# Optimization experiments

Measured on AMD Instinct MI355X. Metric: run time of the kernel, lower is better.

The kernel has to match this reference:

```python
import jax, jax.numpy as jnp
import numpy as np
import itertools

N_PARTICLES = 8388608
GRID_RES = 2048
BOX_SIZE = 1000.0

def _rotations_47():
    perms = list(itertools.permutations([0, 1, 2]))
    signs = list(itertools.product([1, -1], repeat=3))
    mats = []
    for s in signs:
        for p in perms:
            M = np.zeros((3, 3), np.float32)
            M[0, p[0]] = s[0]; M[1, p[1]] = s[1]; M[2, p[2]] = s[2]
            mats.append(M)
    return jnp.asarray(np.stack(mats)[1:])  # drop identity -> 47 matrices

# Analytic stand-ins for jax_cosmo background quantities (EdS-like forms).
def _Gp(a):
    return a ** 1.5

def _dGfa(a):
    return 1.5 * jnp.sqrt(a)

def _a_of_chi(chi):
    return 1.0 / (1.0 + chi / 3000.0)

def _paint_2d(pos, center, width, box_size, res):
    """CIC scatter of particles inside a z-slab onto a [res,res] density plane."""
    z = pos[:, 2]
    sel = ((z >= center - width * 0.5) & (z < center + width * 0.5)).astype(pos.dtype)
    xy = pos[:, :2] * (res / box_size)          # grid coordinates, [N,2]
    i0 = jnp.floor(xy)
    f = xy - i0                                  # CIC fractional offsets
    i0 = i0.astype(jnp.int32)
    ix0 = jnp.mod(i0[:, 0], res); iy0 = jnp.mod(i0[:, 1], res)
    ix1 = jnp.mod(i0[:, 0] + 1, res); iy1 = jnp.mod(i0[:, 1] + 1, res)
    fx, fy = f[:, 0], f[:, 1]
    flat = jnp.zeros((res * res,), dtype=pos.dtype)
    flat = flat.at[ix0 * res + iy0].add(sel * (1 - fx) * (1 - fy))
    flat = flat.at[ix1 * res + iy0].add(sel * fx * (1 - fy))
    flat = flat.at[ix0 * res + iy1].add(sel * (1 - fx) * fy)
    flat = flat.at[ix1 * res + iy1].add(sel * fx * fy)
    return flat.reshape(res, res)

def setup_inputs():
    key = jax.random.key(0)
    k1, k2 = jax.random.split(key)
    positions = jax.random.uniform(k1, (N_PARTICLES, 3), jnp.float32) * BOX_SIZE
    velocities = jax.random.normal(k2, (N_PARTICLES, 3), jnp.float32) * 2.0
    return {
        "positions": positions,
        "velocities": velocities,
        "rotations": _rotations_47(),
        "observer": jnp.zeros((3,), jnp.float32),
        "r_centers": jnp.asarray([250.0, 750.0, 1250.0, 1750.0], jnp.float32),
        "density_widths": jnp.full((4,), 500.0, jnp.float32),
        "t": jnp.float32(0.8),
        "max_comoving_distance": jnp.float32(BOX_SIZE),
        "box_size": jnp.float32(BOX_SIZE),
        "shell_idx": 2,
        "rotation_idx": 1,
        "grid_res": GRID_RES,
    }

def reference(positions, velocities, rotations, observer, r_centers, density_widths,
              t, max_comoving_distance, box_size, shell_idx, rotation_idx, grid_res):
    r_center = r_centers[shell_idx]
    width = density_widths[shell_idx]
    inside_box = r_center + width * 0.5 <= max_comoving_distance

    def inside_branch(args):
        pos, _vel = args
        return _paint_2d(pos, r_center, width, box_size, grid_res)

    def telephoto_branch(args):
        pos, vel = args
        M = rotations[rotation_idx % 47]                                   # [3,3]
        shift = jnp.floor(r_center / max_comoving_distance) * max_comoving_distance
        p_rot = (pos - observer) @ M.T                                      # rotate about observer
        z_axis = jnp.array([0.0, 0.0, 1.0], pos.dtype)
        p_shift = p_rot + z_axis * shift
        v_rot = vel @ M.T
        dist = jnp.linalg.norm(p_shift - observer, axis=-1)                 # [N]
        a_tgt = _a_of_chi(dist)[:, None]                                    # per-particle target scale factor
        ac = jnp.sqrt(t * a_tgt)
        drift = (_Gp(a_tgt) - _Gp(t)) / _dGfa(ac)
        p_drift = p_shift + drift * v_rot
        return _paint_2d(p_drift + observer, r_center, width, box_size, grid_res)

    return jax.lax.cond(inside_box, inside_branch, telephoto_branch, (positions, velocities))
```

## Files before the change

kernel.cpp:

```cpp
#include <hip/hip_runtime.h>
#include <cmath>


#define TSZ    128
#define NBKT   256
#define NXCC   8
#define CAP    4096
#define DEPTH  32
#define NTH    256
#define NBLK   1024
#define VEC    4
#define DESCMAX 512

typedef float vf4 __attribute__((ext_vector_type(4)));

__device__ __forceinline__ int get_xcc_id() {
    int x = __builtin_amdgcn_s_getreg((3 << 11) | (0 << 6) | 20);
    return x & (NXCC - 1);
}

__device__ __forceinline__ float fast_rcp(float x)  { return __builtin_amdgcn_rcpf(x); }
__device__ __forceinline__ float fast_sqrt(float x) { return __builtin_amdgcn_sqrtf(x); }

__device__ __forceinline__ int wrap_idx(int v, int res) {
    v += (v < 0) ? res : 0;
    v += (v < 0) ? res : 0;
    v += (v < 0) ? res : 0;
    v -= (v >= res) ? res : 0;
    v -= (v >= res) ? res : 0;
    v -= (v >= res) ? res : 0;
    if (v < 0 || v >= res) { v %= res; if (v < 0) v += res; }
    return v;
}

__device__ __forceinline__ void scatter_direct(float* __restrict__ out, int res,
                                               int gx0, int gy0, float fx, float fy) {
    int gx1 = gx0 + 1; if (gx1 >= res) gx1 = 0;
    int gy1 = gy0 + 1; if (gy1 >= res) gy1 = 0;
    atomicAdd(&out[gx0 * res + gy0], (1.0f - fx) * (1.0f - fy));
    atomicAdd(&out[gx1 * res + gy0], fx * (1.0f - fy));
    atomicAdd(&out[gx0 * res + gy1], (1.0f - fx) * fy);
    atomicAdd(&out[gx1 * res + gy1], fx * fy);
}

__device__ __forceinline__ void rec_decode(unsigned rec, int b, int tiles,
                                           int& gx, int& gy, float& fx, float& fy) {
    int tx = b / tiles, ty = b - tx * tiles;
    gx = (tx << 7) + (int)(rec >> 25);
    gy = (ty << 7) + (int)((rec >> 18) & 127u);
    fx = (float)((rec >> 9) & 511u) * (1.0f / 512.0f);
    fy = (float)(rec & 511u) * (1.0f / 512.0f);
}

struct Uni {
    float m00, m01, m02, m10, m11, m12, m20, m21, m22;
    float ox, oy, oz, shift;
    float r_lo, r_hi, t, gp_t, scale;
    int   resm1, res, tiles;
    bool  inside;
};

__device__ __forceinline__ void tp_process(
    const Uni& u, float px, float py, float pz, float vx, float vy, float vz,
    unsigned* __restrict__ fill, unsigned* __restrict__ buf,
    float* __restrict__ out)
{
    float X, Y, Z;
    if (u.inside) {
        X = px; Y = py; Z = pz;
    } else {
        const float qx_ = px - u.ox, qy_ = py - u.oy, qz_ = pz - u.oz;
        float rx = u.m00 * qx_ + u.m01 * qy_ + u.m02 * qz_;
        float ry = u.m10 * qx_ + u.m11 * qy_ + u.m12 * qz_;
        float rz = u.m20 * qx_ + u.m21 * qy_ + u.m22 * qz_ + u.shift;

        const float vrx = u.m00 * vx + u.m01 * vy + u.m02 * vz;
        const float vry = u.m10 * vx + u.m11 * vy + u.m12 * vz;
        const float vrz = u.m20 * vx + u.m21 * vy + u.m22 * vz;

        const float dx = rx - u.ox, dy = ry - u.oy, dz = rz - u.oz;
        const float dist  = fast_sqrt(dx * dx + dy * dy + dz * dz);
        const float a_tgt = fast_rcp(1.0f + dist * (1.0f / 3000.0f));
        const float ac    = fast_sqrt(u.t * a_tgt);
        const float gp_a  = a_tgt * fast_sqrt(a_tgt);
        const float drift = (gp_a - u.gp_t) * fast_rcp(1.5f * fast_sqrt(ac));

        X = rx + drift * vrx + u.ox;
        Y = ry + drift * vry + u.oy;
        Z = rz + drift * vrz + u.oz;
    }
    if (!(Z >= u.r_lo && Z < u.r_hi)) return;

    const float gx = X * u.scale, gy = Y * u.scale;
    const float fgx = floorf(gx), fgy = floorf(gy);
    const float fx = gx - fgx, fy = gy - fgy;
    const int ix0 = ((int)fgx) & u.resm1;
    const int iy0 = ((int)fgy) & u.resm1;
    const int st = (ix0 >> 7) * u.tiles + (iy0 >> 7);

    unsigned qx = (unsigned)(fx * 512.0f + 0.5f); if (qx > 511u) qx = 511u;
    unsigned qy = (unsigned)(fy * 512.0f + 0.5f); if (qy > 511u) qy = 511u;
    const unsigned rec = ((unsigned)(ix0 & 127) << 25) | ((unsigned)(iy0 & 127) << 18)
                       | (qx << 9) | qy;

    unsigned p = atomicAdd(&fill[st], 1u);
    if (p < DEPTH) buf[st * DEPTH + p] = rec;
    else { atomicSub(&fill[st], 1u); scatter_direct(out, u.res, ix0, iy0, fx, fy); }
}

__global__ __launch_bounds__(NTH) void tp_bin(
    const float* __restrict__ pos, const float* __restrict__ vel,
    const float* __restrict__ rotations, const float* __restrict__ observer,
    const float* __restrict__ r_centers, const float* __restrict__ widths,
    const float* __restrict__ t_p, const float* __restrict__ maxd_p,
    const float* __restrict__ box_p, const int* __restrict__ shell_p,
    const int* __restrict__ ridx_p,
    unsigned* __restrict__ gcnt, unsigned* __restrict__ grec,
    float* __restrict__ out, int res, int tiles, int n, int rounds)
{
    __shared__ unsigned fill[NBKT];
    __shared__ unsigned buf[NBKT * DEPTH];
    __shared__ unsigned descB[DESCMAX];
    __shared__ unsigned descD[DESCMAX];
    __shared__ unsigned ndesc;

    const int tid = threadIdx.x;
    for (int b = tid; b < NBKT; b += NTH) fill[b] = 0;
    if (tid == 0) ndesc = 0;

    Uni u;
    {
        const int   shell    = shell_p[0];
        const float r_center = r_centers[shell];
        const float width    = widths[shell];
        const float maxd     = maxd_p[0];
        const float box      = box_p[0];
        u.t      = t_p[0];
        u.inside = (r_center + width * 0.5f) <= maxd;
        int ridx = ridx_p[0] % 47; if (ridx < 0) ridx += 47;
        const float* M = rotations + 9 * ridx;
        u.m00 = M[0]; u.m01 = M[1]; u.m02 = M[2];
        u.m10 = M[3]; u.m11 = M[4]; u.m12 = M[5];
        u.m20 = M[6]; u.m21 = M[7]; u.m22 = M[8];
        u.ox = observer[0]; u.oy = observer[1]; u.oz = observer[2];
        u.shift = floorf(r_center / maxd) * maxd;
        u.r_lo = r_center - width * 0.5f;
        u.r_hi = r_center + width * 0.5f;
        u.gp_t = u.t * sqrtf(u.t);
        u.scale = (float)res / box;
        u.resm1 = res - 1; u.res = res; u.tiles = tiles;
    }

    const int xcc = get_xcc_id();
    const int segbase = xcc * NBKT;
    const vf4* __restrict__ pos4 = (const vf4*)pos;
    const vf4* __restrict__ vel4 = (const vf4*)vel;

    __syncthreads();

    for (int r = 0; r < rounds; ++r) {
        const int base = ((r * NBLK + blockIdx.x) * NTH + tid) * VEC;
        if (base + VEC <= n) {
            const int q = base * 3 / 4;
            const vf4 a = __builtin_nontemporal_load(pos4 + q);
            const vf4 b = __builtin_nontemporal_load(pos4 + q + 1);
            const vf4 c = __builtin_nontemporal_load(pos4 + q + 2);
            if (u.inside) {
                tp_process(u, a.x, a.y, a.z, 0, 0, 0, fill, buf, out);
                tp_process(u, a.w, b.x, b.y, 0, 0, 0, fill, buf, out);
                tp_process(u, b.z, b.w, c.x, 0, 0, 0, fill, buf, out);
                tp_process(u, c.y, c.z, c.w, 0, 0, 0, fill, buf, out);
            } else {
                const vf4 d = __builtin_nontemporal_load(vel4 + q);
                const vf4 e = __builtin_nontemporal_load(vel4 + q + 1);
                const vf4 f = __builtin_nontemporal_load(vel4 + q + 2);
                tp_process(u, a.x, a.y, a.z, d.x, d.y, d.z, fill, buf, out);
                tp_process(u, a.w, b.x, b.y, d.w, e.x, e.y, fill, buf, out);
                tp_process(u, b.z, b.w, c.x, e.z, e.w, f.x, fill, buf, out);
                tp_process(u, c.y, c.z, c.w, f.y, f.z, f.w, fill, buf, out);
            }
        } else {
            for (int p = 0; p < VEC; ++p) {
                const int i = base + p;
                if (i < n)
                    tp_process(u, pos[3 * i], pos[3 * i + 1], pos[3 * i + 2],
                               vel[3 * i], vel[3 * i + 1], vel[3 * i + 2],
                               fill, buf, out);
            }
        }
        __syncthreads();
        if (tid < NBKT) {
            const unsigned c = fill[tid];
            const unsigned k = c >> 4;
            if (k) {
                unsigned gbase = atomicAdd(&gcnt[segbase + tid], 16u * k);
                unsigned d = atomicAdd(&ndesc, k);
                for (unsigned g = 0; g < k; ++g) {
                    descB[d + g] = (unsigned)tid | ((g * 16u) << 16);
                    descD[d + g] = gbase + 16u * g;
                }
            }
        }
        __syncthreads();
        const unsigned nd = ndesc;
        for (unsigned did = (unsigned)(tid >> 4); did < nd; did += NTH / 16) {
            const unsigned e = descB[did];
            const unsigned b = e & 0xffffu, so = e >> 16;
            const unsigned dst = descD[did] + (unsigned)(tid & 15);
            const unsigned rv = buf[b * DEPTH + so + (tid & 15)];
            if (dst < CAP) {
                grec[(size_t)(segbase + b) * CAP + dst] = rv;
            } else {
                int gx0, gy0; float ffx, ffy;
                rec_decode(rv, (int)b, u.tiles, gx0, gy0, ffx, ffy);
                scatter_direct(out, u.res, gx0, gy0, ffx, ffy);
            }
        }
        __syncthreads();
        if (tid < NBKT) {
            const unsigned c = fill[tid];
            const unsigned k = c >> 4;
            if (k) {
                const unsigned resid = c - 16u * k;
                for (unsigned j = 0; j < resid; ++j)
                    buf[tid * DEPTH + j] = buf[tid * DEPTH + 16u * k + j];
                fill[tid] = resid;
            }
        }
        if (tid == 0) ndesc = 0;
        __syncthreads();
    }

    if (tid < NBKT) {
        const unsigned c = fill[tid];
        if (c) {
            unsigned d = atomicAdd(&ndesc, 1u);
            unsigned gbase = atomicAdd(&gcnt[segbase + tid], c);
            descB[d] = (unsigned)tid | (c << 16);
            descD[d] = gbase;
        }
    }
    __syncthreads();
    const unsigned nd = ndesc;
    for (unsigned did = (unsigned)(tid >> 4); did < nd; did += NTH / 16) {
        const unsigned e = descB[did];
        const unsigned b = e & 0xffffu, c = e >> 16;
        const unsigned lane = (unsigned)(tid & 15);
        if (lane < c) {
            const unsigned dst = descD[did] + lane;
            const unsigned rv = buf[b * DEPTH + lane];
            if (dst < CAP) {
                grec[(size_t)(segbase + b) * CAP + dst] = rv;
            } else {
                int gx0, gy0; float ffx, ffy;
                rec_decode(rv, (int)b, u.tiles, gx0, gy0, ffx, ffy);
                scatter_direct(out, u.res, gx0, gy0, ffx, ffy);
            }
        }
    }
}

__global__ __launch_bounds__(1024) void tp_paint(
    const unsigned* __restrict__ gcnt, const unsigned* __restrict__ grec,
    float* __restrict__ out, int res, int tiles)
{
    __shared__ unsigned long long quad[4][64 * 64];
    const int b = blockIdx.x;
    const int tx = b / tiles, ty = b - tx * tiles;

    for (int c = threadIdx.x; c < 4 * 64 * 64; c += blockDim.x)
        quad[c >> 12][c & 4095] = 0ull;
    __syncthreads();

    for (int x = 0; x < NXCC; ++x) {
        unsigned m = gcnt[x * NBKT + b]; if (m > CAP) m = CAP;
        const unsigned* rr = grec + (size_t)(x * NBKT + b) * CAP;
        for (unsigned k = threadIdx.x; k < m; k += blockDim.x) {
            const unsigned p = rr[k];
            const int li = (int)(p >> 25);
            const int lj = (int)((p >> 18) & 127u);
            const unsigned qx = (p >> 9) & 511u;
            const unsigned qy = p & 511u;
            const unsigned ax = 512u - qx, ay = 512u - qy;
            const unsigned long long w00 = (ax * ay + 128u) >> 8;
            const unsigned long long w01 = (ax * qy + 128u) >> 8;
            const unsigned long long w10 = (qx * ay + 128u) >> 8;
            const unsigned long long w11 = (qx * qy + 128u) >> 8;
            const unsigned long long pk = w00 | (w01 << 16) | (w10 << 32) | (w11 << 48);
            const int g = ((li & 1) << 1) | (lj & 1);
            atomicAdd(&quad[g][(li >> 1) * 64 + (lj >> 1)], pk);
        }
    }
    __syncthreads();

    for (int c = threadIdx.x; c < (TSZ + 1) * (TSZ + 1); c += blockDim.x) {
        const int i = c / (TSZ + 1), j = c - i * (TSZ + 1);
        unsigned acc = 0;
        #pragma unroll
        for (int r = 0; r < 2; ++r) {
            const int ii = i - r;
            if (ii < 0 || ii > TSZ - 1) continue;
            #pragma unroll
            for (int s = 0; s < 2; ++s) {
                const int jj = j - s;
                if (jj < 0 || jj > TSZ - 1) continue;
                const int g = ((ii & 1) << 1) | (jj & 1);
                const unsigned long long v = quad[g][(ii >> 1) * 64 + (jj >> 1)];
                acc += (unsigned)((v >> (16 * (r * 2 + s))) & 0xffffull);
            }
        }
        const float val = (float)acc * (1.0f / 1024.0f);
        int gx = tx * TSZ + i; if (gx >= res) gx -= res;
        int gy = ty * TSZ + j; if (gy >= res) gy -= res;
        float* dst = &out[gx * res + gy];
        if (i == 0 || j == 0 || i == TSZ || j == TSZ) {
            if (val != 0.0f) atomicAdd(dst, val);
        } else {
            *dst += val;
        }
    }
}

__global__ __launch_bounds__(256) void tp_direct(
    const float* __restrict__ pos, const float* __restrict__ vel,
    const float* __restrict__ rotations, const float* __restrict__ observer,
    const float* __restrict__ r_centers, const float* __restrict__ widths,
    const float* __restrict__ t_p, const float* __restrict__ maxd_p,
    const float* __restrict__ box_p, const int* __restrict__ shell_p,
    const int* __restrict__ ridx_p, float* __restrict__ out, int res, int n)
{
    int i = blockIdx.x * blockDim.x + threadIdx.x;
    if (i >= n) return;
    const int   shell    = shell_p[0];
    const float r_center = r_centers[shell];
    const float width    = widths[shell];
    const float maxd     = maxd_p[0];
    const float box      = box_p[0];
    const float t        = t_p[0];
    const bool  inside   = (r_center + width * 0.5f) <= maxd;
    int ridx = ridx_p[0] % 47; if (ridx < 0) ridx += 47;

    float px = pos[3 * i], py = pos[3 * i + 1], pz = pos[3 * i + 2];
    float X, Y, Z;
    if (inside) {
        X = px; Y = py; Z = pz;
    } else {
        const float* M = rotations + 9 * ridx;
        const float ox = observer[0], oy = observer[1], oz = observer[2];
        const float qx = px - ox, qy = py - oy, qz = pz - oz;
        float rx = M[0] * qx + M[1] * qy + M[2] * qz;
        float ry = M[3] * qx + M[4] * qy + M[5] * qz;
        float rz = M[6] * qx + M[7] * qy + M[8] * qz + floorf(r_center / maxd) * maxd;
        const float vx = vel[3 * i], vy = vel[3 * i + 1], vz = vel[3 * i + 2];
        const float vrx = M[0] * vx + M[1] * vy + M[2] * vz;
        const float vry = M[3] * vx + M[4] * vy + M[5] * vz;
        const float vrz = M[6] * vx + M[7] * vy + M[8] * vz;
        const float dx = rx - ox, dy = ry - oy, dz = rz - oz;
        const float dist  = sqrtf(dx * dx + dy * dy + dz * dz);
        const float a_tgt = 1.0f / (1.0f + dist / 3000.0f);
        const float ac    = sqrtf(t * a_tgt);
        const float drift = (a_tgt * sqrtf(a_tgt) - t * sqrtf(t)) / (1.5f * sqrtf(ac));
        X = rx + drift * vrx + ox;
        Y = ry + drift * vry + oy;
        Z = rz + drift * vrz + oz;
    }
    if (!(Z >= r_center - width * 0.5f && Z < r_center + width * 0.5f)) return;

    const float scale = (float)res / box;
    const float gx = X * scale, gy = Y * scale;
    const float fgx = floorf(gx), fgy = floorf(gy);
    scatter_direct(out, res, wrap_idx((int)fgx, res), wrap_idx((int)fgy, res),
                   gx - fgx, gy - fgy);
}

extern "C" void kernel_launch(void* const* d_in, const int* in_sizes, int n_in,
                              void* d_out, int out_size, void* d_ws, size_t ws_size,
                              hipStream_t stream) {
    const float* pos   = (const float*)d_in[0];
    const float* velv  = (const float*)d_in[1];
    const float* rot   = (const float*)d_in[2];
    const float* obs   = (const float*)d_in[3];
    const float* rc    = (const float*)d_in[4];
    const float* dw    = (const float*)d_in[5];
    const float* t     = (const float*)d_in[6];
    const float* maxd  = (const float*)d_in[7];
    const float* box   = (const float*)d_in[8];
    const int*   shell = (const int*)d_in[9];
    const int*   ridx  = (const int*)d_in[10];
    float* out = (float*)d_out;

    const int n   = in_sizes[0] / 3;
    const int res = (int)llround(sqrt((double)out_size));

    hipMemsetAsync(out, 0, (size_t)out_size * sizeof(float), stream);

    const int tiles = res / TSZ;
    const int nt2 = tiles * tiles;
    const size_t cnt_bytes = (size_t)NXCC * NBKT * sizeof(unsigned);
    const size_t rec_bytes = (size_t)NXCC * NBKT * CAP * sizeof(unsigned);
    const bool pow2 = res > 0 && (res & (res - 1)) == 0;

    if (!pow2 || res % TSZ != 0 || nt2 > NBKT ||
        (long long)res * res != (long long)out_size ||
        ws_size < cnt_bytes + rec_bytes) {
        tp_direct<<<(n + 255) / 256, 256, 0, stream>>>(
            pos, velv, rot, obs, rc, dw, t, maxd, box, shell, ridx, out, res, n);
        return;
    }

    unsigned* gcnt = (unsigned*)d_ws;
    unsigned* grec = (unsigned*)((char*)d_ws + cnt_bytes);

    hipMemsetAsync(gcnt, 0, cnt_bytes, stream);

    const int per_round = NBLK * NTH * VEC;
    const int rounds = (n + per_round - 1) / per_round;
    tp_bin<<<NBLK, NTH, 0, stream>>>(
        pos, velv, rot, obs, rc, dw, t, maxd, box, shell, ridx,
        gcnt, grec, out, res, tiles, n, rounds);

    tp_paint<<<nt2, 1024, 0, stream>>>(gcnt, grec, out, res, tiles);
}
```

Baseline: 283.8 us.

## Route bin overflow records through a global overflow list consumed by paint

Records that overflow a block's shared bucket or the per-tile global capacity are now appended to a global overflow list instead of being atomically scattered into the output grid. Each paint block scans the whole list and folds matching records into its shared accumulator. When nothing spilled past the list's capacity, the paint kernel writes interior cells with a plain store instead of a read-modify-write. This removes scattered global float atomics during binning. In exchange, every paint block scans the full list, and the list counter is one global atomic that all blocks contend on.

```diff
diff --git a/kernel.cpp b/kernel.cpp
--- a/kernel.cpp
+++ b/kernel.cpp
@@ -5,12 +5,13 @@
 #define TSZ    128
 #define NBKT   256
 #define NXCC   8
-#define CAP    4096
+#define CAP    4016
 #define DEPTH  32
 #define NTH    256
 #define NBLK   1024
 #define VEC    4
 #define DESCMAX 512
+#define OVFMAX 65536
 
 typedef float vf4 __attribute__((ext_vector_type(4)));
 
@@ -63,6 +64,7 @@
 __device__ __forceinline__ void tp_process(
     const Uni& u, float px, float py, float pz, float vx, float vy, float vz,
     unsigned* __restrict__ fill, unsigned* __restrict__ buf,
+    unsigned* __restrict__ ovfcnt, unsigned long long* __restrict__ ovf,
     float* __restrict__ out)
 {
     float X, Y, Z;
@@ -105,7 +107,12 @@
 
     unsigned p = atomicAdd(&fill[st], 1u);
     if (p < DEPTH) buf[st * DEPTH + p] = rec;
-    else { atomicSub(&fill[st], 1u); scatter_direct(out, u.res, ix0, iy0, fx, fy); }
+    else {
+        atomicSub(&fill[st], 1u);
+        const unsigned idx = atomicAdd(ovfcnt, 1u);
+        if (idx < OVFMAX) ovf[idx] = ((unsigned long long)(unsigned)st << 32) | rec;
+        else scatter_direct(out, u.res, ix0, iy0, fx, fy);
+    }
 }
 
 __global__ __launch_bounds__(NTH) void tp_bin(
@@ -116,6 +123,7 @@
     const float* __restrict__ box_p, const int* __restrict__ shell_p,
     const int* __restrict__ ridx_p,
     unsigned* __restrict__ gcnt, unsigned* __restrict__ grec,
+    unsigned* __restrict__ ovfcnt, unsigned long long* __restrict__ ovf,
     float* __restrict__ out, int res, int tiles, int n, int rounds)
 {
     __shared__ unsigned fill[NBKT];
@@ -166,18 +174,18 @@
             const vf4 b = __builtin_nontemporal_load(pos4 + q + 1);
             const vf4 c = __builtin_nontemporal_load(pos4 + q + 2);
             if (u.inside) {
-                tp_process(u, a.x, a.y, a.z, 0, 0, 0, fill, buf, out);
-                tp_process(u, a.w, b.x, b.y, 0, 0, 0, fill, buf, out);
-                tp_process(u, b.z, b.w, c.x, 0, 0, 0, fill, buf, out);
-                tp_process(u, c.y, c.z, c.w, 0, 0, 0, fill, buf, out);
+                tp_process(u, a.x, a.y, a.z, 0, 0, 0, fill, buf, ovfcnt, ovf, out);
+                tp_process(u, a.w, b.x, b.y, 0, 0, 0, fill, buf, ovfcnt, ovf, out);
+                tp_process(u, b.z, b.w, c.x, 0, 0, 0, fill, buf, ovfcnt, ovf, out);
+                tp_process(u, c.y, c.z, c.w, 0, 0, 0, fill, buf, ovfcnt, ovf, out);
             } else {
                 const vf4 d = __builtin_nontemporal_load(vel4 + q);
                 const vf4 e = __builtin_nontemporal_load(vel4 + q + 1);
                 const vf4 f = __builtin_nontemporal_load(vel4 + q + 2);
-                tp_process(u, a.x, a.y, a.z, d.x, d.y, d.z, fill, buf, out);
-                tp_process(u, a.w, b.x, b.y, d.w, e.x, e.y, fill, buf, out);
-                tp_process(u, b.z, b.w, c.x, e.z, e.w, f.x, fill, buf, out);
-                tp_process(u, c.y, c.z, c.w, f.y, f.z, f.w, fill, buf, out);
+                tp_process(u, a.x, a.y, a.z, d.x, d.y, d.z, fill, buf, ovfcnt, ovf, out);
+                tp_process(u, a.w, b.x, b.y, d.w, e.x, e.y, fill, buf, ovfcnt, ovf, out);
+                tp_process(u, b.z, b.w, c.x, e.z, e.w, f.x, fill, buf, ovfcnt, ovf, out);
+                tp_process(u, c.y, c.z, c.w, f.y, f.z, f.w, fill, buf, ovfcnt, ovf, out);
             }
         } else {
             for (int p = 0; p < VEC; ++p) {
@@ -185,7 +193,7 @@
                 if (i < n)
                     tp_process(u, pos[3 * i], pos[3 * i + 1], pos[3 * i + 2],
                                vel[3 * i], vel[3 * i + 1], vel[3 * i + 2],
-                               fill, buf, out);
+                               fill, buf, ovfcnt, ovf, out);
             }
         }
         __syncthreads();
@@ -211,9 +219,13 @@
             if (dst < CAP) {
                 grec[(size_t)(segbase + b) * CAP + dst] = rv;
             } else {
-                int gx0, gy0; float ffx, ffy;
-                rec_decode(rv, (int)b, u.tiles, gx0, gy0, ffx, ffy);
-                scatter_direct(out, u.res, gx0, gy0, ffx, ffy);
+                const unsigned idx = atomicAdd(ovfcnt, 1u);
+                if (idx < OVFMAX) ovf[idx] = ((unsigned long long)b << 32) | rv;
+                else {
+                    int gx0, gy0; float ffx, ffy;
+                    rec_decode(rv, (int)b, u.tiles, gx0, gy0, ffx, ffy);
+                    scatter_direct(out, u.res, gx0, gy0, ffx, ffy);
+                }
             }
         }
         __syncthreads();
@@ -252,9 +264,13 @@
             if (dst < CAP) {
                 grec[(size_t)(segbase + b) * CAP + dst] = rv;
             } else {
-                int gx0, gy0; float ffx, ffy;
-                rec_decode(rv, (int)b, u.tiles, gx0, gy0, ffx, ffy);
-                scatter_direct(out, u.res, gx0, gy0, ffx, ffy);
+                const unsigned idx = atomicAdd(ovfcnt, 1u);
+                if (idx < OVFMAX) ovf[idx] = ((unsigned long long)b << 32) | rv;
+                else {
+                    int gx0, gy0; float ffx, ffy;
+                    rec_decode(rv, (int)b, u.tiles, gx0, gy0, ffx, ffy);
+                    scatter_direct(out, u.res, gx0, gy0, ffx, ffy);
+                }
             }
         }
     }
@@ -262,6 +278,7 @@
 
 __global__ __launch_bounds__(1024) void tp_paint(
     const unsigned* __restrict__ gcnt, const unsigned* __restrict__ grec,
+    const unsigned* __restrict__ ovfcnt, const unsigned long long* __restrict__ ovf,
     float* __restrict__ out, int res, int tiles)
 {
     __shared__ unsigned long long quad[4][64 * 64];
@@ -291,6 +308,28 @@
             atomicAdd(&quad[g][(li >> 1) * 64 + (lj >> 1)], pk);
         }
     }
+
+    const unsigned ovfn_raw = ovfcnt[0];
+    const bool accum = ovfn_raw > OVFMAX;
+    const unsigned ovfn = accum ? (unsigned)OVFMAX : ovfn_raw;
+    for (unsigned k = threadIdx.x; k < ovfn; k += blockDim.x) {
+        const unsigned long long e = ovf[k];
+        if ((unsigned)(e >> 32) == (unsigned)b) {
+            const unsigned p = (unsigned)e;
+            const int li = (int)(p >> 25);
+            const int lj = (int)((p >> 18) & 127u);
+            const unsigned qx = (p >> 9) & 511u;
+            const unsigned qy = p & 511u;
+            const unsigned ax = 512u - qx, ay = 512u - qy;
+            const unsigned long long w00 = (ax * ay + 128u) >> 8;
+            const unsigned long long w01 = (ax * qy + 128u) >> 8;
+            const unsigned long long w10 = (qx * ay + 128u) >> 8;
+            const unsigned long long w11 = (qx * qy + 128u) >> 8;
+            const unsigned long long pk = w00 | (w01 << 16) | (w10 << 32) | (w11 << 48);
+            const int g = ((li & 1) << 1) | (lj & 1);
+            atomicAdd(&quad[g][(li >> 1) * 64 + (lj >> 1)], pk);
+        }
+    }
     __syncthreads();
 
     for (int c = threadIdx.x; c < (TSZ + 1) * (TSZ + 1); c += blockDim.x) {
@@ -315,8 +354,10 @@
         float* dst = &out[gx * res + gy];
         if (i == 0 || j == 0 || i == TSZ || j == TSZ) {
             if (val != 0.0f) atomicAdd(dst, val);
+        } else if (accum) {
+            *dst += val;
         } else {
-            *dst += val;
+            *dst = val;
         }
     }
 }
@@ -397,27 +438,30 @@
     const int tiles = res / TSZ;
     const int nt2 = tiles * tiles;
     const size_t cnt_bytes = (size_t)NXCC * NBKT * sizeof(unsigned);
+    const size_t ovf_bytes = 16 + (size_t)OVFMAX * 8;
     const size_t rec_bytes = (size_t)NXCC * NBKT * CAP * sizeof(unsigned);
     const bool pow2 = res > 0 && (res & (res - 1)) == 0;
 
     if (!pow2 || res % TSZ != 0 || nt2 > NBKT ||
         (long long)res * res != (long long)out_size ||
-        ws_size < cnt_bytes + rec_bytes) {
+        ws_size < cnt_bytes + ovf_bytes + rec_bytes) {
         tp_direct<<<(n + 255) / 256, 256, 0, stream>>>(
             pos, velv, rot, obs, rc, dw, t, maxd, box, shell, ridx, out, res, n);
         return;
     }
 
     unsigned* gcnt = (unsigned*)d_ws;
-    unsigned* grec = (unsigned*)((char*)d_ws + cnt_bytes);
-
-    hipMemsetAsync(gcnt, 0, cnt_bytes, stream);
+    unsigned* ovfcnt = (unsigned*)((char*)d_ws + cnt_bytes);
+    unsigned long long* ovf = (unsigned long long*)((char*)d_ws + cnt_bytes + 16);
+    unsigned* grec = (unsigned*)((char*)d_ws + cnt_bytes + ovf_bytes);
+
+    hipMemsetAsync(gcnt, 0, cnt_bytes + 16, stream);
 
     const int per_round = NBLK * NTH * VEC;
     const int rounds = (n + per_round - 1) / per_round;
     tp_bin<<<NBLK, NTH, 0, stream>>>(
         pos, velv, rot, obs, rc, dw, t, maxd, box, shell, ridx,
-        gcnt, grec, out, res, tiles, n, rounds);
-
-    tp_paint<<<nt2, 1024, 0, stream>>>(gcnt, grec, out, res, tiles);
-}
+        gcnt, grec, ovfcnt, ovf, out, res, tiles, n, rounds);
+
+    tp_paint<<<nt2, 1024, 0, stream>>>(gcnt, grec, ovfcnt, ovf, out, res, tiles);
+}
```

New measurement: 280.8 us. About the same (-1.1%).
